# Kernel tuning notes

Measured on AMD Instinct MI355X. Metric: run time of the kernel, lower is better.

Reference implementation:

```python
import jax, jax.numpy as jnp
import numpy as np

NH = 12  # num_heads


def _rms(y, g, eps=1e-6):
    # RMSNorm over the full model dim (applied before the head reshape, as in the source)
    return y * jax.lax.rsqrt(jnp.mean(y * y, axis=-1, keepdims=True) + eps) * g


def _rope(t, cos, sin, total_len):
    # t: [B, S, n, d]; rotate first total_len tokens, pass the tail through unchanged
    b, s, n, d = t.shape
    c = d // 2
    tm = t[:, :total_len].reshape(b, total_len, n, c, 2)
    tr, ti = tm[..., 0], tm[..., 1]
    co = cos[None, :, None, :]
    si = sin[None, :, None, :]
    rot = jnp.stack([tr * co - ti * si, tr * si + ti * co], axis=-1).reshape(b, total_len, n, d)
    if total_len < s:
        return jnp.concatenate([rot, t[:, total_len:]], axis=1)
    return rot


def setup_inputs() -> dict:
    key = jax.random.key(0)
    ks = jax.random.split(key, 8)
    B, F, H, W = 4, 4, 16, 28
    S = F * H * W  # 1792 tokens
    D = 1536
    d = D // NH    # 128
    c = d // 2     # 64
    MAXSEQ = 64
    x = jax.random.normal(ks[0], (B, S, D), jnp.float32)
    seq_lens = jnp.full((B,), S, dtype=jnp.int32)
    grid_sizes = jnp.tile(jnp.array([[F, H, W]], dtype=jnp.int32), (B, 1))
    ang = jnp.arange(MAXSEQ, dtype=jnp.float32)[:, None] * (
        10000.0 ** (-jnp.arange(c, dtype=jnp.float32) / c))[None, :]
    w = lambda k, shp: jax.random.normal(k, shp, jnp.float32) * 0.02
    return {
        "x": x,
        "seq_lens": seq_lens,
        "grid_sizes": grid_sizes,
        "freqs_cos": jnp.cos(ang),
        "freqs_sin": jnp.sin(ang),
        "Wq": w(ks[1], (D, D)), "bq": jnp.zeros((D,), jnp.float32),
        "Wk": w(ks[2], (D, D)), "bk": jnp.zeros((D,), jnp.float32),
        "Wv": w(ks[3], (D, D)), "bv": jnp.zeros((D,), jnp.float32),
        "Wo": w(ks[4], (D, D)), "bo": jnp.zeros((D,), jnp.float32),
        "gq": jnp.ones((D,), jnp.float32),
        "gk": jnp.ones((D,), jnp.float32),
        "num_modalities": 1,
    }


def reference(x, seq_lens, grid_sizes, freqs_cos, freqs_sin,
              Wq, bq, Wk, bk, Wv, bv, Wo, bo, gq, gk, num_modalities):
    b, s, D = x.shape
    d = D // NH
    c = d // 2
    # QKV projections + RMSNorm on q/k (norm over the full dim, then split heads)
    q = _rms(x @ Wq.T + bq, gq).reshape(b, s, NH, d)
    k = _rms(x @ Wk.T + bk, gk).reshape(b, s, NH, d)
    v = (x @ Wv.T + bv).reshape(b, s, NH, d)
    # grid metadata is static (same grid for all samples in this setup)
    f, h, w = (int(z) for z in np.asarray(grid_sizes)[0])
    m = int(num_modalities)
    ct = c - 2 * (c // 3)
    ch = c // 3
    seq_per = f * h * w
    total_len = min(seq_per * m, s)

    def grid_freqs(fr):
        # build per-token (t,h,w) frequency table: [seq_per, c], tiled over modalities
        ft = jnp.broadcast_to(fr[:f, :ct][:, None, None, :], (f, h, w, ct))
        fh = jnp.broadcast_to(fr[:h, ct:ct + ch][None, :, None, :], (f, h, w, ch))
        fw = jnp.broadcast_to(fr[:w, ct + ch:c][None, None, :, :], (f, h, w, ch))
        base = jnp.concatenate([ft, fh, fw], axis=-1).reshape(seq_per, c)
        return jnp.tile(base, (m, 1))[:total_len]

    cos = grid_freqs(freqs_cos)
    sin = grid_freqs(freqs_sin)
    q = _rope(q, cos, sin, total_len)
    k = _rope(k, cos, sin, total_len)
    # full (window_size=(-1,-1)) attention with k_lens masking
    scale = 1.0 / jnp.sqrt(jnp.float32(d))
    scores = jnp.einsum('bqhd,bkhd->bhqk', q, k) * scale
    kmask = jnp.arange(s)[None, :] < seq_lens[:, None]  # [B, S]
    scores = jnp.where(kmask[:, None, None, :], scores, jnp.float32(-1e30))
    attn = jax.nn.softmax(scores, axis=-1)
    out = jnp.einsum('bhqk,bkhd->bqhd', attn, v).reshape(b, s, D)
    return out @ Wo.T + bo
```

## Files before the change

### kernel.cpp

```cpp
#include <hip/hip_runtime.h>
#include <hip/hip_bf16.h>

typedef short bf16x8 __attribute__((ext_vector_type(8)));
typedef float f32x4 __attribute__((ext_vector_type(4)));
typedef float f32x16 __attribute__((ext_vector_type(16)));

#define NH 12
#define SEQ 1792
#define DMODEL 1536
#define HD 128

static __device__ __forceinline__ void gload16(const void* g, void* l) {
  __builtin_amdgcn_global_load_lds((const __attribute__((address_space(1))) void*)g,
                                   (__attribute__((address_space(3))) void*)l, 16, 0, 0);
}

static __device__ __forceinline__ short f2bf(float x) {
  __hip_bfloat16 h = __float2bfloat16(x);
  return *reinterpret_cast<short*>(&h);
}

static __device__ __forceinline__ unsigned pack2(float lo, float hi) {
  unsigned a = (unsigned)(unsigned short)f2bf(lo);
  unsigned b = (unsigned)(unsigned short)f2bf(hi);
  return a | (b << 16);
}

__global__ __launch_bounds__(256) void cast_all_kernel(
    const float* __restrict__ x, const float* __restrict__ wq, const float* __restrict__ wk,
    const float* __restrict__ wv, const float* __restrict__ wo,
    __hip_bfloat16* __restrict__ xb, __hip_bfloat16* __restrict__ wb,
    __hip_bfloat16* __restrict__ wob) {
  int i = blockIdx.x * 256 + threadIdx.x;
  const float* src; __hip_bfloat16* dst; int j;
  if (i < 2752512)      { src = x;  dst = xb;            j = i; }
  else if (i < 3342336) { src = wq; dst = wb;            j = i - 2752512; }
  else if (i < 3932160) { src = wk; dst = wb + 2359296;  j = i - 3342336; }
  else if (i < 4521984) { src = wv; dst = wb + 4718592;  j = i - 3932160; }
  else if (i < 5111808) { src = wo; dst = wob;           j = i - 4521984; }
  else return;
  float4 v = reinterpret_cast<const float4*>(src)[j];
  short4 r;
  r.x = f2bf(v.x); r.y = f2bf(v.y); r.z = f2bf(v.z); r.w = f2bf(v.w);
  reinterpret_cast<short4*>(dst)[j] = r;
}

template<int MODE>
__global__ __launch_bounds__(512, 2) void gemm8(
    const __hip_bfloat16* __restrict__ A, const __hip_bfloat16* __restrict__ B,
    int nN, int cpx,
    const float* __restrict__ bq, const float* __restrict__ bk, const float* __restrict__ bv,
    __hip_bfloat16* __restrict__ qbuf, __hip_bfloat16* __restrict__ kbuf,
    __hip_bfloat16* __restrict__ vt,
    const float* __restrict__ bo, float* __restrict__ outp)
{
  constexpr int K = DMODEL;
  constexpr int nT = K / 64;
  constexpr int nIt = nT / 2;
  __shared__ char LDSRAW[131072];
  const int tid = threadIdx.x;
  const int l = tid & 63, w = tid >> 6;
  const int lr = l & 15, lg = l >> 4;
  const int wr = w >> 2, wc = w & 3;

  const int orig = blockIdx.x;
  const int wg = (orig & 7) * cpx + (orig >> 3);
  const int m0 = (wg / nN) * 256, n0 = (wg % nN) * 256;

  const int hrow0 = tid >> 3;
  const int scb0 = ((tid & 7) << 4) ^ ((hrow0 & 7) << 4);

  auto stageA = [&](int t, int half) {
    const char* s = (const char*)(A + (size_t)(m0 + half * 128) * K + t * 64);
    char* d = LDSRAW + (t & 1) * 32768 + half * 16384;
    gload16(s + (size_t)hrow0 * (K * 2) + scb0, d + tid * 16);
    gload16(s + (size_t)(hrow0 + 64) * (K * 2) + scb0, d + (tid + 512) * 16);
  };
  auto stageB = [&](int t, int half) {
    const char* s = (const char*)(B + (size_t)(n0 + half * 128) * K + t * 64);
    char* d = LDSRAW + 65536 + (t & 1) * 32768 + half * 16384;
    gload16(s + (size_t)hrow0 * (K * 2) + scb0, d + tid * 16);
    gload16(s + (size_t)(hrow0 + 64) * (K * 2) + scb0, d + (tid + 512) * 16);
  };

  f32x4 acc[8][4] = {};
  bf16x8 afr0[4][2], afr1[4][2], b0e[2][2], b0o[2][2], b1f[2][2];

  auto RA = [&](int p, int mh, bf16x8 (&dst)[4][2]) {
    const char* base = LDSRAW + p * 32768 + wr * 16384;
#pragma unroll
    for (int i = 0; i < 4; ++i) {
      int hrow = (mh * 4 + i) * 16 + lr;
#pragma unroll
      for (int ks = 0; ks < 2; ++ks)
        dst[i][ks] = *reinterpret_cast<const bf16x8*>(
            base + hrow * 128 + ((ks * 64 + lg * 16) ^ ((hrow & 7) << 4)));
    }
  };
  auto RB = [&](int p, int nh, bf16x8 (&dst)[2][2]) {
#pragma unroll
    for (int j = 0; j < 2; ++j) {
      int cbase = wc * 64 + (nh * 2 + j) * 16;
      int half = cbase >> 7;
      int hrow = (cbase & 127) + lr;
      const char* base = LDSRAW + 65536 + p * 32768 + half * 16384;
#pragma unroll
      for (int ks = 0; ks < 2; ++ks)
        dst[j][ks] = *reinterpret_cast<const bf16x8*>(
            base + hrow * 128 + ((ks * 64 + lg * 16) ^ ((hrow & 7) << 4)));
    }
  };
  auto MF = [&](int mh, int nh, bf16x8 (&a)[4][2], bf16x8 (&b)[2][2]) {
    __builtin_amdgcn_s_setprio(1);
#pragma unroll
    for (int i = 0; i < 4; ++i)
#pragma unroll
      for (int j = 0; j < 2; ++j)
#pragma unroll
        for (int ks = 0; ks < 2; ++ks)
          acc[mh * 4 + i][nh * 2 + j] = __builtin_amdgcn_mfma_f32_16x16x32_bf16(
              a[i][ks], b[j][ks], acc[mh * 4 + i][nh * 2 + j], 0, 0, 0);
    __builtin_amdgcn_s_setprio(0);
  };

#define SB0 __builtin_amdgcn_sched_barrier(0)
#define BAR __builtin_amdgcn_s_barrier()
#define TILE(p, t, b0c, b0n)                                                 \
  { RB(p, 1, b1f);                                                           \
    if ((t) + 1 < nT) stageA((t) + 1, 1);                                    \
    SB0;                                                                     \
    MF(0, 0, afr0, b0c);                                                     \
    BAR;                                                                     \
    RA(p, 1, afr1);                                                          \
    if ((t) + 1 < nT) stageB((t) + 1, 0);                                    \
    SB0;                                                                     \
    MF(0, 1, afr0, b1f);                                                     \
    BAR;                                                                     \
    if ((t) + 1 < nT) stageB((t) + 1, 1);                                    \
    if ((t) + 2 < nT) stageA((t) + 2, 0);                                    \
    SB0;                                                                     \
    MF(1, 1, afr1, b1f);                                                     \
    if ((t) + 2 < nT) asm volatile("s_waitcnt vmcnt(2)" ::: "memory");       \
    else              asm volatile("s_waitcnt vmcnt(0)" ::: "memory");       \
    BAR;                                                                     \
    if ((t) + 1 < nT) { RA((p) ^ 1, 0, afr0); RB((p) ^ 1, 0, b0n); }         \
    SB0;                                                                     \
    MF(1, 0, afr1, b0c);                                                     \
    BAR;                                                                     \
  }

  stageA(0, 0); stageA(0, 1); stageB(0, 0); stageB(0, 1); stageA(1, 0);
  asm volatile("s_waitcnt vmcnt(2)" ::: "memory");
  BAR;
  RA(0, 0, afr0); RB(0, 0, b0e);

  for (int it2 = 0; it2 < nIt; ++it2) {
    TILE(0, 2 * it2, b0e, b0o);
    TILE(1, 2 * it2 + 1, b0o, b0e);
  }
#undef TILE
#undef SB0
#undef BAR

  if (MODE == 0) {
    const int which = n0 / DMODEL;
    if (which < 2) {
#pragma unroll
      for (int fj = 0; fj < 4; ++fj) {
        int ncol = n0 + wc * 64 + fj * 16 + lr;
        int cc = ncol - which * DMODEL;
        int hh = cc >> 7, dd = cc & 127;
        float bias = (which == 0 ? bq : bk)[cc];
#pragma unroll
        for (int fi = 0; fi < 8; ++fi)
#pragma unroll
          for (int r = 0; r < 4; ++r) {
            int rowg = m0 + wr * 128 + fi * 16 + lg * 4 + r;
            int bbb = rowg / SEQ;
            int sr = rowg - bbb * SEQ;
            __hip_bfloat16 hv = __float2bfloat16(acc[fi][fj][r] + bias);
            if (which == 0)
              qbuf[(((size_t)(bbb * NH + hh)) * SEQ + sr) * HD + dd] = hv;
            else
              kbuf[(((size_t)(bbb * NH + hh)) * SEQ + sr) * HD + dd] = hv;
          }
      }
    } else {
      __syncthreads();
      const int cc0 = n0 - 2 * DMODEL;
#pragma unroll
      for (int fj = 0; fj < 4; ++fj) {
        int d_loc = wc * 64 + fj * 16 + lr;
        float bias = bv[cc0 + d_loc];
#pragma unroll
        for (int fi = 0; fi < 8; ++fi)
#pragma unroll
          for (int r = 0; r < 4; ++r) {
            int s_loc = wr * 128 + fi * 16 + lg * 4 + r;
            *reinterpret_cast<short*>(LDSRAW + d_loc * 512 +
                ((s_loc * 2) ^ ((d_loc & 7) << 4))) = f2bf(acc[fi][fj][r] + bias);
          }
      }
      __syncthreads();
      const int bbb = m0 / SEQ;
      const int sr0 = m0 - bbb * SEQ;
#pragma unroll
      for (int c = 0; c < 16; ++c) {
        int g = c * 512 + tid;
        int d = g >> 5;
        int sb = (g & 31) << 4;
        bf16x8 vvv = *reinterpret_cast<const bf16x8*>(
            LDSRAW + d * 512 + (sb ^ ((d & 7) << 4)));
        int ddg = cc0 + d, hh = ddg >> 7, dd = ddg & 127;
        *reinterpret_cast<bf16x8*>(
            &vt[(((size_t)(bbb * NH + hh)) * HD + dd) * SEQ + sr0 + (sb >> 1)]) = vvv;
      }
    }
  } else {
#pragma unroll
    for (int fj = 0; fj < 4; ++fj) {
      int ncol = n0 + wc * 64 + fj * 16 + lr;
      float bias = bo[ncol];
#pragma unroll
      for (int fi = 0; fi < 8; ++fi)
#pragma unroll
        for (int r = 0; r < 4; ++r) {
          int rowg = m0 + wr * 128 + fi * 16 + lg * 4 + r;
          outp[(size_t)rowg * DMODEL + ncol] = acc[fi][fj][r] + bias;
        }
    }
  }
}

__global__ __launch_bounds__(256) void rmsrope_kernel(
    __hip_bfloat16* __restrict__ qb, __hip_bfloat16* __restrict__ kb,
    const float* __restrict__ gq, const float* __restrict__ gk,
    const float* __restrict__ fc, const float* __restrict__ fs,
    const int* __restrict__ gsz, const int* __restrict__ nmod)
{
  const int bs = blockIdx.x;
  const int b = bs / SEQ, s = bs - b * SEQ;
  const int t = threadIdx.x;
  const int f = gsz[0], h = gsz[1], wd = gsz[2];
  const int mm = nmod[0];
  const int seq_per = f * h * wd;
  int total_len = seq_per * mm; if (total_len > SEQ) total_len = SEQ;
  const bool dorope = s < total_len;
  int fi = 0, hi2 = 0, wi = 0;
  if (dorope) {
    int p = s % seq_per;
    fi = p / (h * wd);
    int rem = p - fi * (h * wd);
    hi2 = rem / wd;
    wi = rem - hi2 * wd;
  }
  float qv[3][2], kv[3][2];
  float sq = 0.f, sk = 0.f;
#pragma unroll
  for (int r = 0; r < 3; ++r) {
    int pi = t + r * 256;
    int head = pi >> 6;
    int dd = (pi & 63) * 2;
    size_t addr = (((size_t)(b * NH + head)) * SEQ + s) * HD + dd;
    __hip_bfloat162 q2 = *reinterpret_cast<const __hip_bfloat162*>(&qb[addr]);
    __hip_bfloat162 k2 = *reinterpret_cast<const __hip_bfloat162*>(&kb[addr]);
    qv[r][0] = __bfloat162float(q2.x); qv[r][1] = __bfloat162float(q2.y);
    kv[r][0] = __bfloat162float(k2.x); kv[r][1] = __bfloat162float(k2.y);
    sq += qv[r][0] * qv[r][0] + qv[r][1] * qv[r][1];
    sk += kv[r][0] * kv[r][0] + kv[r][1] * kv[r][1];
  }
#pragma unroll
  for (int off = 1; off < 64; off <<= 1) {
    sq += __shfl_xor(sq, off);
    sk += __shfl_xor(sk, off);
  }
  __shared__ float red[2][4];
  if ((t & 63) == 0) { red[0][t >> 6] = sq; red[1][t >> 6] = sk; }
  __syncthreads();
  float tq = red[0][0] + red[0][1] + red[0][2] + red[0][3];
  float tk = red[1][0] + red[1][1] + red[1][2] + red[1][3];
  float rq = rsqrtf(tq * (1.0f / DMODEL) + 1e-6f);
  float rk = rsqrtf(tk * (1.0f / DMODEL) + 1e-6f);
  const float scale = 0.08838834764831845f;
#pragma unroll
  for (int r = 0; r < 3; ++r) {
    int pi = t + r * 256;
    int head = pi >> 6;
    int dd = (pi & 63) * 2;
    int col = pi * 2;
    size_t addr = (((size_t)(b * NH + head)) * SEQ + s) * HD + dd;
    float q0 = qv[r][0] * rq * gq[col], q1 = qv[r][1] * rq * gq[col + 1];
    float k0 = kv[r][0] * rk * gk[col], k1 = kv[r][1] * rk * gk[col + 1];
    if (dorope) {
      int j = pi & 63;
      int row = (j < 22) ? fi : (j < 43) ? hi2 : wi;
      float co = fc[row * 64 + j], si = fs[row * 64 + j];
      float a;
      a = q0 * co - q1 * si; q1 = q0 * si + q1 * co; q0 = a;
      a = k0 * co - k1 * si; k1 = k0 * si + k1 * co; k0 = a;
    }
    q0 *= scale; q1 *= scale;
    __hip_bfloat162 oq, ok;
    oq.x = __float2bfloat16(q0); oq.y = __float2bfloat16(q1);
    ok.x = __float2bfloat16(k0); ok.y = __float2bfloat16(k1);
    *reinterpret_cast<__hip_bfloat162*>(&qb[addr]) = oq;
    *reinterpret_cast<__hip_bfloat162*>(&kb[addr]) = ok;
  }
}

__global__ __launch_bounds__(256, 2) void attn_kernel(
    const __hip_bfloat16* __restrict__ qb, const __hip_bfloat16* __restrict__ kbuf,
    const __hip_bfloat16* __restrict__ vt, const int* __restrict__ seq_lens,
    __hip_bfloat16* __restrict__ ob)
{
  const int orig = blockIdx.x;
  const int wg = (orig & 7) * 84 + (orig >> 3);
  const int bh = wg / 14, qt = wg % 14;
  const int bbb = bh / NH, hh = bh - bbb * NH;
  const int tid = threadIdx.x;
  const int w = tid >> 6, l = tid & 63;
  const int lq = l & 31, h = l >> 5;
  const int sl = seq_lens[bbb];
  const __hip_bfloat16* Q = qb + (size_t)bh * SEQ * HD;
  const char* Kc = (const char*)(kbuf + (size_t)bh * SEQ * HD);
  const __hip_bfloat16* Vp = vt + (size_t)bh * HD * SEQ;
  const int q0 = qt * 128 + w * 32;

  __shared__ __hip_bfloat16 Kt[2][64 * 128];
  __shared__ __hip_bfloat16 Vt[128 * 64];

  bf16x8 qf[8];
#pragma unroll
  for (int kc = 0; kc < 8; ++kc)
    qf[kc] = *reinterpret_cast<const bf16x8*>(
        &Q[(size_t)(q0 + lq) * HD + kc * 16 + h * 8]);

  f32x16 oacc[4] = {};
  float m = -3e38f, ll = 0.f;

  const int nkt = (sl + 63) >> 6;

  auto stageK = [&](int buf, int k0) {
    char* Lb = (char*)&Kt[buf][0];
#pragma unroll
    for (int q2 = 0; q2 < 4; ++q2) {
      int chunk = q2 * 256 + tid;
      int row = chunk >> 4;
      int cb = (chunk & 15) << 4;
      int scb = cb ^ ((row & 7) << 4);
      gload16(Kc + (size_t)(k0 + row) * 256 + scb, Lb + chunk * 16);
    }
  };
  auto stageV = [&](int k0) {
    char* Lb = (char*)&Vt[0];
#pragma unroll
    for (int q2 = 0; q2 < 4; ++q2) {
      int chunk = q2 * 256 + tid;
      int row = chunk >> 3;
      int cb = (chunk & 7) << 4;
      int scb = cb ^ ((row & 7) << 4);
      gload16(Vp + (size_t)row * SEQ + k0 + (scb >> 1), Lb + chunk * 16);
    }
  };

  stageK(0, 0);
  for (int kt = 0; kt < nkt; ++kt) {
    __syncthreads();
    const int k0 = kt * 64;
    stageV(k0);
    const bool pf = (kt + 1 < nkt);
    if (pf) stageK((kt + 1) & 1, k0 + 64);
    const char* Kl = (const char*)&Kt[kt & 1][0];
    const char* Vl = (const char*)&Vt[0];

    f32x16 sa[2] = {};
#pragma unroll
    for (int cb = 0; cb < 2; ++cb) {
      int row = cb * 32 + lq;
      int swz = (row & 7) << 4;
#pragma unroll
      for (int kc = 0; kc < 8; ++kc) {
        bf16x8 kf = *reinterpret_cast<const bf16x8*>(
            Kl + row * 256 + ((kc * 32 + h * 16) ^ swz));
        sa[cb] = __builtin_amdgcn_mfma_f32_32x32x16_bf16(kf, qf[kc], sa[cb], 0, 0, 0);
      }
    }

    if (k0 + 64 > sl) {
#pragma unroll
      for (int cb = 0; cb < 2; ++cb)
#pragma unroll
        for (int r = 0; r < 16; ++r) {
          int kg = k0 + cb * 32 + (r & 3) + 8 * (r >> 2) + 4 * h;
          if (kg >= sl) sa[cb][r] = -3e38f;
        }
    }

    float mx = -3e38f;
#pragma unroll
    for (int cb = 0; cb < 2; ++cb)
#pragma unroll
      for (int r = 0; r < 16; ++r) mx = fmaxf(mx, sa[cb][r]);
    mx = fmaxf(mx, __shfl_xor(mx, 32));

    if (__any(mx - m > 8.f)) {
      float mn = fmaxf(m, mx);
      float alpha = __expf(m - mn);
      m = mn;
      ll *= alpha;
#pragma unroll
      for (int r = 0; r < 16; ++r) {
        float ar = __shfl(alpha, (r & 3) + 8 * (r >> 2) + 4 * h);
#pragma unroll
        for (int d0 = 0; d0 < 4; ++d0) oacc[d0][r] *= ar;
      }
    }

    float rs = 0.f;
#pragma unroll
    for (int cb = 0; cb < 2; ++cb)
#pragma unroll
      for (int r = 0; r < 16; ++r) {
        float e = __expf(sa[cb][r] - m);
        sa[cb][r] = e;
        rs += e;
      }
    rs += __shfl_xor(rs, 32);
    ll += rs;

    if (pf) asm volatile("s_waitcnt vmcnt(4)" ::: "memory");
    else    asm volatile("s_waitcnt vmcnt(0)" ::: "memory");
    __builtin_amdgcn_s_barrier();

#pragma unroll
    for (int c = 0; c < 4; ++c) {
      const int cb = c >> 1, r0 = 8 * (c & 1);
      unsigned A01 = pack2(sa[cb][r0],     sa[cb][r0 + 1]);
      unsigned A23 = pack2(sa[cb][r0 + 2], sa[cb][r0 + 3]);
      unsigned B01 = pack2(sa[cb][r0 + 4], sa[cb][r0 + 5]);
      unsigned B23 = pack2(sa[cb][r0 + 6], sa[cb][r0 + 7]);
      unsigned s1 = __shfl_xor(h ? A01 : B01, 32);
      unsigned s2 = __shfl_xor(h ? A23 : B23, 32);
      int4 wv;
      wv.x = (int)(h ? s1 : A01);
      wv.y = (int)(h ? s2 : A23);
      wv.z = (int)(h ? B01 : s1);
      wv.w = (int)(h ? B23 : s2);
      bf16x8 pa = *reinterpret_cast<bf16x8*>(&wv);
#pragma unroll
      for (int d0 = 0; d0 < 4; ++d0) {
        int vr = d0 * 32 + lq;
        bf16x8 vv = *reinterpret_cast<const bf16x8*>(
            Vl + vr * 128 + ((c * 32 + h * 16) ^ ((vr & 7) << 4)));
        oacc[d0] = __builtin_amdgcn_mfma_f32_32x32x16_bf16(pa, vv, oacc[d0], 0, 0, 0);
      }
    }
  }

  float invl = 1.0f / ll;
#pragma unroll
  for (int r = 0; r < 16; ++r) {
    int qoff = (r & 3) + 8 * (r >> 2) + 4 * h;
    float ir = __shfl(invl, qoff);
    int qrow = q0 + qoff;
#pragma unroll
    for (int d0 = 0; d0 < 4; ++d0)
      ob[((size_t)bbb * SEQ + qrow) * DMODEL + hh * HD + d0 * 32 + lq] =
          __float2bfloat16(oacc[d0][r] * ir);
  }
}

extern "C" void kernel_launch(void* const* d_in, const int* in_sizes, int n_in,
                              void* d_out, int out_size, void* d_ws, size_t ws_size,
                              hipStream_t stream) {
  const float* x   = (const float*)d_in[0];
  const int* seq_lens   = (const int*)d_in[1];
  const int* grid_sizes = (const int*)d_in[2];
  const float* fc  = (const float*)d_in[3];
  const float* fs  = (const float*)d_in[4];
  const float* Wq  = (const float*)d_in[5];
  const float* bq  = (const float*)d_in[6];
  const float* Wk  = (const float*)d_in[7];
  const float* bk  = (const float*)d_in[8];
  const float* Wv  = (const float*)d_in[9];
  const float* bv  = (const float*)d_in[10];
  const float* Wo  = (const float*)d_in[11];
  const float* bo  = (const float*)d_in[12];
  const float* gq  = (const float*)d_in[13];
  const float* gk  = (const float*)d_in[14];
  const int* nmod  = (const int*)d_in[15];
  float* out = (float*)d_out;

  char* ws = (char*)d_ws;
  __hip_bfloat16* xb   = (__hip_bfloat16*)(ws + 0);
  __hip_bfloat16* wb   = (__hip_bfloat16*)(ws + 22020096);
  __hip_bfloat16* wob  = (__hip_bfloat16*)(ws + 36175872);
  __hip_bfloat16* qbuf = (__hip_bfloat16*)(ws + 40894464);
  __hip_bfloat16* kbuf = (__hip_bfloat16*)(ws + 62914560);
  __hip_bfloat16* vtb  = (__hip_bfloat16*)(ws + 84934656);
  __hip_bfloat16* ob   = xb;

  cast_all_kernel<<<(5111808 + 255) / 256, 256, 0, stream>>>(x, Wq, Wk, Wv, Wo, xb, wb, wob);

  gemm8<0><<<504, 512, 0, stream>>>(xb, wb, 18, 63, bq, bk, bv,
                                    qbuf, kbuf, vtb, nullptr, nullptr);
  rmsrope_kernel<<<7168, 256, 0, stream>>>(qbuf, kbuf, gq, gk, fc, fs, grid_sizes, nmod);
  attn_kernel<<<672, 256, 0, stream>>>(qbuf, kbuf, vtb, seq_lens, ob);
  gemm8<1><<<168, 512, 0, stream>>>(ob, wob, 6, 21, nullptr, nullptr, nullptr,
                                    nullptr, nullptr, nullptr, bo, out);
}
```

Baseline: 319.6 us.

## Replace 256x256 ping-pong GEMM with simpler 256x128 tile, 4-wave GEMM

Swaps the hand-scheduled 512-thread 256x256 GEMM, which used a K=64 step and fine-grained barrier interleaving, for a 256-thread 256x128 tile with a K=32 step and a plain double-buffered loop. This doubles the block count and halves LDS use so more blocks fit per CU. In exchange it drops the explicit overlap of loads with MFMA and adds a full barrier on every K step. It also simplifies the epilogue index math by assuming a 256-row tile never crosses a batch boundary.

```diff
diff --git a/kernel.cpp b/kernel.cpp
--- a/kernel.cpp
+++ b/kernel.cpp
@@ -46,7 +46,7 @@
 }
 
 template<int MODE>
-__global__ __launch_bounds__(512, 2) void gemm8(
+__global__ __launch_bounds__(256, 2) void gemm_km(
     const __hip_bfloat16* __restrict__ A, const __hip_bfloat16* __restrict__ B,
     int nN, int cpx,
     const float* __restrict__ bq, const float* __restrict__ bk, const float* __restrict__ bv,
@@ -55,115 +55,72 @@
     const float* __restrict__ bo, float* __restrict__ outp)
 {
   constexpr int K = DMODEL;
-  constexpr int nT = K / 64;
-  constexpr int nIt = nT / 2;
-  __shared__ char LDSRAW[131072];
+  constexpr int nT = K / 32;
+  __shared__ char LDSRAW[65536];
   const int tid = threadIdx.x;
   const int l = tid & 63, w = tid >> 6;
   const int lr = l & 15, lg = l >> 4;
-  const int wr = w >> 2, wc = w & 3;
+  const int wr = w >> 1, wc = w & 1;
 
   const int orig = blockIdx.x;
   const int wg = (orig & 7) * cpx + (orig >> 3);
-  const int m0 = (wg / nN) * 256, n0 = (wg % nN) * 256;
-
-  const int hrow0 = tid >> 3;
-  const int scb0 = ((tid & 7) << 4) ^ ((hrow0 & 7) << 4);
-
-  auto stageA = [&](int t, int half) {
-    const char* s = (const char*)(A + (size_t)(m0 + half * 128) * K + t * 64);
-    char* d = LDSRAW + (t & 1) * 32768 + half * 16384;
-    gload16(s + (size_t)hrow0 * (K * 2) + scb0, d + tid * 16);
-    gload16(s + (size_t)(hrow0 + 64) * (K * 2) + scb0, d + (tid + 512) * 16);
+  const int m0 = (wg / nN) * 256, n0 = (wg % nN) * 128;
+
+  auto stage = [&](int t) {
+    char* Ad = LDSRAW + (t & 1) * 16384;
+    char* Bd = LDSRAW + 32768 + (t & 1) * 8192;
+#pragma unroll
+    for (int c4 = 0; c4 < 4; ++c4) {
+      int chunk = c4 * 256 + tid;
+      int row = chunk >> 2;
+      int scol = ((chunk & 3) << 4) ^ ((row & 3) << 4);
+      gload16((const char*)A + (size_t)(m0 + row) * (K * 2) + t * 64 + scol,
+              Ad + chunk * 16);
+    }
+#pragma unroll
+    for (int c2 = 0; c2 < 2; ++c2) {
+      int chunk = c2 * 256 + tid;
+      int row = chunk >> 2;
+      int scol = ((chunk & 3) << 4) ^ ((row & 3) << 4);
+      gload16((const char*)B + (size_t)(n0 + row) * (K * 2) + t * 64 + scol,
+              Bd + chunk * 16);
+    }
   };
-  auto stageB = [&](int t, int half) {
-    const char* s = (const char*)(B + (size_t)(n0 + half * 128) * K + t * 64);
-    char* d = LDSRAW + 65536 + (t & 1) * 32768 + half * 16384;
-    gload16(s + (size_t)hrow0 * (K * 2) + scb0, d + tid * 16);
-    gload16(s + (size_t)(hrow0 + 64) * (K * 2) + scb0, d + (tid + 512) * 16);
-  };
 
   f32x4 acc[8][4] = {};
-  bf16x8 afr0[4][2], afr1[4][2], b0e[2][2], b0o[2][2], b1f[2][2];
-
-  auto RA = [&](int p, int mh, bf16x8 (&dst)[4][2]) {
-    const char* base = LDSRAW + p * 32768 + wr * 16384;
-#pragma unroll
-    for (int i = 0; i < 4; ++i) {
-      int hrow = (mh * 4 + i) * 16 + lr;
-#pragma unroll
-      for (int ks = 0; ks < 2; ++ks)
-        dst[i][ks] = *reinterpret_cast<const bf16x8*>(
-            base + hrow * 128 + ((ks * 64 + lg * 16) ^ ((hrow & 7) << 4)));
-    }
-  };
-  auto RB = [&](int p, int nh, bf16x8 (&dst)[2][2]) {
-#pragma unroll
-    for (int j = 0; j < 2; ++j) {
-      int cbase = wc * 64 + (nh * 2 + j) * 16;
-      int half = cbase >> 7;
-      int hrow = (cbase & 127) + lr;
-      const char* base = LDSRAW + 65536 + p * 32768 + half * 16384;
-#pragma unroll
-      for (int ks = 0; ks < 2; ++ks)
-        dst[j][ks] = *reinterpret_cast<const bf16x8*>(
-            base + hrow * 128 + ((ks * 64 + lg * 16) ^ ((hrow & 7) << 4)));
-    }
-  };
-  auto MF = [&](int mh, int nh, bf16x8 (&a)[4][2], bf16x8 (&b)[2][2]) {
+
+  stage(0);
+  for (int t = 0; t < nT; ++t) {
+    __syncthreads();
+    if (t + 1 < nT) stage(t + 1);
+    const char* Al = LDSRAW + (t & 1) * 16384;
+    const char* Bl = LDSRAW + 32768 + (t & 1) * 8192;
+    bf16x8 afr[8], bfr[4];
+#pragma unroll
+    for (int fi = 0; fi < 8; ++fi) {
+      int row = wr * 128 + fi * 16 + lr;
+      afr[fi] = *reinterpret_cast<const bf16x8*>(
+          Al + row * 64 + ((lg * 16) ^ ((row & 3) << 4)));
+    }
+#pragma unroll
+    for (int fj = 0; fj < 4; ++fj) {
+      int row = wc * 64 + fj * 16 + lr;
+      bfr[fj] = *reinterpret_cast<const bf16x8*>(
+          Bl + row * 64 + ((lg * 16) ^ ((row & 3) << 4)));
+    }
     __builtin_amdgcn_s_setprio(1);
 #pragma unroll
-    for (int i = 0; i < 4; ++i)
-#pragma unroll
-      for (int j = 0; j < 2; ++j)
-#pragma unroll
-        for (int ks = 0; ks < 2; ++ks)
-          acc[mh * 4 + i][nh * 2 + j] = __builtin_amdgcn_mfma_f32_16x16x32_bf16(
-              a[i][ks], b[j][ks], acc[mh * 4 + i][nh * 2 + j], 0, 0, 0);
+    for (int fi = 0; fi < 8; ++fi)
+#pragma unroll
+      for (int fj = 0; fj < 4; ++fj)
+        acc[fi][fj] = __builtin_amdgcn_mfma_f32_16x16x32_bf16(afr[fi], bfr[fj], acc[fi][fj], 0, 0, 0);
     __builtin_amdgcn_s_setprio(0);
-  };
-
-#define SB0 __builtin_amdgcn_sched_barrier(0)
-#define BAR __builtin_amdgcn_s_barrier()
-#define TILE(p, t, b0c, b0n)                                                 \
-  { RB(p, 1, b1f);                                                           \
-    if ((t) + 1 < nT) stageA((t) + 1, 1);                                    \
-    SB0;                                                                     \
-    MF(0, 0, afr0, b0c);                                                     \
-    BAR;                                                                     \
-    RA(p, 1, afr1);                                                          \
-    if ((t) + 1 < nT) stageB((t) + 1, 0);                                    \
-    SB0;                                                                     \
-    MF(0, 1, afr0, b1f);                                                     \
-    BAR;                                                                     \
-    if ((t) + 1 < nT) stageB((t) + 1, 1);                                    \
-    if ((t) + 2 < nT) stageA((t) + 2, 0);                                    \
-    SB0;                                                                     \
-    MF(1, 1, afr1, b1f);                                                     \
-    if ((t) + 2 < nT) asm volatile("s_waitcnt vmcnt(2)" ::: "memory");       \
-    else              asm volatile("s_waitcnt vmcnt(0)" ::: "memory");       \
-    BAR;                                                                     \
-    if ((t) + 1 < nT) { RA((p) ^ 1, 0, afr0); RB((p) ^ 1, 0, b0n); }         \
-    SB0;                                                                     \
-    MF(1, 0, afr1, b0c);                                                     \
-    BAR;                                                                     \
-  }
-
-  stageA(0, 0); stageA(0, 1); stageB(0, 0); stageB(0, 1); stageA(1, 0);
-  asm volatile("s_waitcnt vmcnt(2)" ::: "memory");
-  BAR;
-  RA(0, 0, afr0); RB(0, 0, b0e);
-
-  for (int it2 = 0; it2 < nIt; ++it2) {
-    TILE(0, 2 * it2, b0e, b0o);
-    TILE(1, 2 * it2 + 1, b0o, b0e);
-  }
-#undef TILE
-#undef SB0
-#undef BAR
+  }
 
   if (MODE == 0) {
     const int which = n0 / DMODEL;
+    const int bbb = m0 / SEQ;
+    const int sr0 = m0 - bbb * SEQ;
     if (which < 2) {
 #pragma unroll
       for (int fj = 0; fj < 4; ++fj) {
@@ -175,9 +132,7 @@
         for (int fi = 0; fi < 8; ++fi)
 #pragma unroll
           for (int r = 0; r < 4; ++r) {
-            int rowg = m0 + wr * 128 + fi * 16 + lg * 4 + r;
-            int bbb = rowg / SEQ;
-            int sr = rowg - bbb * SEQ;
+            int sr = sr0 + wr * 128 + fi * 16 + lg * 4 + r;
             __hip_bfloat16 hv = __float2bfloat16(acc[fi][fj][r] + bias);
             if (which == 0)
               qbuf[(((size_t)(bbb * NH + hh)) * SEQ + sr) * HD + dd] = hv;
@@ -202,16 +157,15 @@
           }
       }
       __syncthreads();
-      const int bbb = m0 / SEQ;
-      const int sr0 = m0 - bbb * SEQ;
+      const int hh = (cc0 >> 7);
 #pragma unroll
       for (int c = 0; c < 16; ++c) {
-        int g = c * 512 + tid;
+        int g = c * 256 + tid;
         int d = g >> 5;
         int sb = (g & 31) << 4;
         bf16x8 vvv = *reinterpret_cast<const bf16x8*>(
             LDSRAW + d * 512 + (sb ^ ((d & 7) << 4)));
-        int ddg = cc0 + d, hh = ddg >> 7, dd = ddg & 127;
+        int dd = (cc0 + d) & 127;
         *reinterpret_cast<bf16x8*>(
             &vt[(((size_t)(bbb * NH + hh)) * HD + dd) * SEQ + sr0 + (sb >> 1)]) = vvv;
       }
@@ -502,10 +456,10 @@
 
   cast_all_kernel<<<(5111808 + 255) / 256, 256, 0, stream>>>(x, Wq, Wk, Wv, Wo, xb, wb, wob);
 
-  gemm8<0><<<504, 512, 0, stream>>>(xb, wb, 18, 63, bq, bk, bv,
-                                    qbuf, kbuf, vtb, nullptr, nullptr);
+  gemm_km<0><<<1008, 256, 0, stream>>>(xb, wb, 36, 126, bq, bk, bv,
+                                       qbuf, kbuf, vtb, nullptr, nullptr);
   rmsrope_kernel<<<7168, 256, 0, stream>>>(qbuf, kbuf, gq, gk, fc, fs, grid_sizes, nmod);
   attn_kernel<<<672, 256, 0, stream>>>(qbuf, kbuf, vtb, seq_lens, ob);
-  gemm8<1><<<168, 512, 0, stream>>>(ob, wob, 6, 21, nullptr, nullptr, nullptr,
-                                    nullptr, nullptr, nullptr, bo, out);
-}
+  gemm_km<1><<<336, 256, 0, stream>>>(ob, wob, 12, 42, nullptr, nullptr, nullptr,
+                                      nullptr, nullptr, nullptr, bo, out);
+}
```

Result: faster. 301.7 us, median of 2 (-5.6%).
